# Optimization experiments

Measured on AMD Instinct MI355X. Metric: run time of the kernel, lower is better.

Reference implementation:

```python
import jax, jax.numpy as jnp
import numpy as np

N = 200000   # node_dim
E = 128      # emb_size
B = 4096     # batch of events
H = 20       # hist_len (neighbor_size)
NEG = 5      # neg_size
SIGMA = 1.0
MAXT = 1.0   # max_d_time
INDEX = 4096.0


def setup_inputs() -> dict:
    key = jax.random.key(0)
    ks = jax.random.split(key, 18)
    inp = dict(
        node_features=jax.random.normal(ks[0], (N, E), jnp.float32),
        sources=jax.random.randint(ks[1], (B,), 0, N),
        destinations=jax.random.randint(ks[2], (B,), 0, N),
        e_times=jax.random.uniform(ks[3], (B,), jnp.float32),
        s_h_nodes=jax.random.randint(ks[4], (B, H), 0, N),
        t_h_nodes=jax.random.randint(ks[5], (B, H), 0, N),
        s_h_times=jax.random.uniform(ks[6], (B, H), jnp.float32),
        t_h_times=jax.random.uniform(ks[7], (B, H), jnp.float32),
        s_mask=(jax.random.uniform(ks[8], (B, H)) < 0.9).astype(jnp.float32),
        t_mask=(jax.random.uniform(ks[9], (B, H)) < 0.9).astype(jnp.float32),
        neg_src=jax.random.randint(ks[10], (B * NEG,), 0, N),
        neg_dst=jax.random.randint(ks[11], (B * NEG,), 0, N),
        # MLP: Linear(E,60) -> ReLU -> Linear(60,E)
        W1=jax.random.normal(ks[12], (E, 60), jnp.float32) * 0.05,
        b1=jnp.zeros((60,), jnp.float32),
        W2=jax.random.normal(ks[13], (60, E), jnp.float32) * 0.05,
        b2=jnp.zeros((E,), jnp.float32),
        # GAT params
        W=jax.random.normal(ks[14], (E, E), jnp.float32) * 0.05,
        a=jax.random.normal(ks[15], (2 * E, 1), jnp.float32) * 0.05,
        delta_s_p=jnp.ones((N,), jnp.float32),
        delta_t_p=jnp.ones((N,), jnp.float32),
        gw=jax.random.normal(ks[16], (E, 1), jnp.float32) * 0.05,
        gb=jnp.zeros((1,), jnp.float32),
    )
    return inp


def _forward(node_features, sources, destinations, e_times, s_h_nodes, t_h_nodes,
             s_h_times, t_h_times, s_mask, t_mask, neg_src, neg_dst,
             W1, b1, W2, b2, W, a, delta_s_p, delta_t_p, gw, gb):
    # MLP node embedding
    node_emb = jnp.maximum(node_features @ W1 + b1, 0.0) @ W2 + b2  # [N,E]

    pos0 = node_emb[sources]        # [B,E]
    pos1 = node_emb[destinations]   # [B,E]
    pos = jax.nn.relu(jnp.sum(pos0 * pos1, axis=1))  # [B]

    neg0 = node_emb[neg_src].reshape(B, NEG, E)
    neg1 = node_emb[neg_dst].reshape(B, NEG, E)
    neg_s = jax.nn.relu(jnp.einsum('be,bne->bn', pos0, neg1))
    neg_t = jax.nn.relu(jnp.einsum('be,bne->bn', pos1, neg0))

    # --- computer_similarity (vectorized over hist_len) ---
    et = e_times / MAXT
    d_s = jnp.abs(et[:, None] - s_h_times / MAXT)   # [B,H]
    d_t = jnp.abs(et[:, None] - t_h_times / MAXT)   # [B,H]
    ds = delta_s_p[sources][:, None]                 # [B,1]
    dt = delta_t_p[destinations][:, None]            # [B,1]

    s_h_emb = node_emb[s_h_nodes]   # [B,H,E]
    t_h_emb = node_emb[t_h_nodes]   # [B,H,E]

    a1, a2 = a[:E, 0], a[E:, 0]
    proj_s = pos0 @ W               # [B,E]
    proj_t = pos1 @ W
    proj_sh = jnp.einsum('bhe,ef->bhf', s_h_emb, W)  # [B,H,E]
    proj_th = jnp.einsum('bhe,ef->bhf', t_h_emb, W)

    score_s = (proj_s @ a1)[:, None] + jnp.einsum('bhe,e->bh', proj_sh, a2)
    score_t = (proj_t @ a1)[:, None] + jnp.einsum('bhe,e->bh', proj_th, a2)
    # NOTE: original code uses delta_s for BOTH branches (bug kept for fidelity)
    sim_s = jax.nn.leaky_relu(jnp.exp(-ds * d_s) * score_s, negative_slope=0.2)
    sim_t = jax.nn.leaky_relu(jnp.exp(-ds * d_t) * score_t, negative_slope=0.2)

    att_s = jax.nn.softmax(sim_s, axis=1)   # [B,H]
    att_t = jax.nn.softmax(sim_t, axis=1)

    s_hat = jnp.sum((att_s * s_mask)[:, :, None] * proj_sh, axis=1)  # [B,E]
    t_hat = jnp.sum((att_t * t_mask)[:, :, None] * proj_th, axis=1)

    g_s = s_hat * jnp.exp(-ds * jnp.mean(d_s, axis=1, keepdims=True))
    g_t = t_hat * jnp.exp(-dt * jnp.mean(d_t, axis=1, keepdims=True))
    stacked = jnp.stack([g_s, g_t], axis=1)                  # [B,2,E]
    glogits = jnp.tanh(stacked @ gw + gb)                    # [B,2,1]
    gatt = jax.nn.softmax(glogits, axis=1)[:, :, 0]          # [B,2]
    ga_s, ga_t = gatt[:, 0], gatt[:, 1]

    p_mu = jnp.sum((pos0 - pos1) ** 2, axis=1)                       # [B]
    p_alpha_s = jnp.sum((s_h_emb - pos1[:, None, :]) ** 2, axis=2)   # [B,H]
    p_alpha_t = jnp.sum((t_h_emb - pos0[:, None, :]) ** 2, axis=2)
    p_lambda = (p_mu
                + ga_s * jnp.sum(att_s * p_alpha_s * jnp.exp(ds * d_s) * s_mask, axis=1)
                + ga_t * jnp.sum(att_t * p_alpha_t * jnp.exp(dt * d_t) * t_mask, axis=1))

    n_mu_s = jnp.sum((pos0[:, None, :] - neg1) ** 2, axis=2)  # [B,NEG]
    n_mu_t = jnp.sum((pos1[:, None, :] - neg0) ** 2, axis=2)
    n_alpha_s = jnp.sum((s_h_emb[:, :, None, :] - neg1[:, None, :, :]) ** 2, axis=3)  # [B,H,NEG]
    n_alpha_t = jnp.sum((t_h_emb[:, :, None, :] - neg0[:, None, :, :]) ** 2, axis=3)
    n_lambda_s = n_mu_s + ga_s[:, None] * jnp.sum(
        att_s[:, :, None] * n_alpha_s * jnp.exp(ds * d_s)[:, :, None] * s_mask[:, :, None], axis=1)
    n_lambda_t = n_mu_t + ga_t[:, None] * jnp.sum(
        att_t[:, :, None] * n_alpha_t * jnp.exp(dt * d_t)[:, :, None] * t_mask[:, :, None], axis=1)

    # --- loss ---
    pos_loss = -jnp.log(jax.nn.sigmoid(p_lambda / SIGMA) + 1e-6) * (pos - 1.0) ** 2
    s_neg_loss = -jnp.log(jax.nn.sigmoid(-n_lambda_s / SIGMA) + 1e-6) * neg_s ** 2
    t_neg_loss = -jnp.log(jax.nn.sigmoid(-n_lambda_t / SIGMA) + 1e-6) * neg_t ** 2
    tgsl_loss = pos_loss.sum() / INDEX + (s_neg_loss.sum() + t_neg_loss.sum()) / (INDEX * NEG)

    estimated_weights = pos  # relu(sum(x0*x1)) same as pos
    return tgsl_loss, estimated_weights, node_emb


def reference(node_features, sources, destinations, e_times, s_h_nodes, t_h_nodes,
              s_h_times, t_h_times, s_mask, t_mask, neg_src, neg_dst,
              W1, b1, W2, b2, W, a, delta_s_p, delta_t_p, gw, gb):
    return _forward(node_features, sources, destinations, e_times, s_h_nodes, t_h_nodes,
                    s_h_times, t_h_times, s_mask, t_mask, neg_src, neg_dst,
                    W1, b1, W2, b2, W, a, delta_s_p, delta_t_p, gw, gb)
```

## Files before the change

kernel.cpp:

```cpp
#include <hip/hip_runtime.h>
#include <hip/hip_bf16.h>
#include <math.h>

#define N_NODES 200000
#define E_DIM   128
#define B_EDGES 4096
#define H_NBRS  20
#define NEG_K   5
#define HID     60
#define Z_ROW   (N_NODES + 3)

typedef short bf16x8 __attribute__((ext_vector_type(8)));
typedef float f32x4  __attribute__((ext_vector_type(4)));

#define MFMA(a, b, c) __builtin_amdgcn_mfma_f32_16x16x32_bf16((a), (b), (c), 0, 0, 0)

__device__ __forceinline__ unsigned short f2b(float f) {
  unsigned u = __float_as_uint(f);
  u += 0x7fffu + ((u >> 16) & 1u);
  return (unsigned short)(u >> 16);
}

__device__ __forceinline__ float wave_sum(float v) {
  #pragma unroll
  for (int m = 1; m < 64; m <<= 1) v += __shfl_xor(v, m, 64);
  return v;
}
__device__ __forceinline__ float wave_max(float v) {
  #pragma unroll
  for (int m = 1; m < 64; m <<= 1) v = fmaxf(v, __shfl_xor(v, m, 64));
  return v;
}

__device__ __forceinline__ bf16x8 xfrag(const unsigned short* xS, int m, int kk, int q) {
  int chunk = (kk * 4 + q) ^ ((m & 3) << 2);
  return *(const bf16x8*)(xS + m * 128 + chunk * 8);
}

__global__ __launch_bounds__(1024) void prep_kernel(
    const float* __restrict__ W, const float* __restrict__ a,
    const float* __restrict__ gw, const float* __restrict__ W1,
    const float* __restrict__ W2, unsigned short* __restrict__ w1f,
    unsigned short* __restrict__ w2f, float* __restrict__ wav,
    unsigned short* __restrict__ embH, float* __restrict__ out_loss) {
  __shared__ float wavS[3 * E_DIM];
  const int tid = threadIdx.x;
  const int lane = tid & 63, grp = tid >> 6;
  const int q = lane >> 4, c = lane & 15;

  {
    const int kk = grp >> 2, t = grp & 3;
    const int n = t * 16 + c, k0 = kk * 32 + q * 8;
    unsigned v[4];
    #pragma unroll
    for (int jj = 0; jj < 4; ++jj) {
      unsigned short lo = (n < 60) ? f2b(W1[(k0 + 2 * jj) * 60 + n]) : 0;
      unsigned short hi = (n < 60) ? f2b(W1[(k0 + 2 * jj + 1) * 60 + n]) : 0;
      v[jj] = (unsigned)lo | ((unsigned)hi << 16);
    }
    ((uint4*)w1f)[grp * 64 + lane] = make_uint4(v[0], v[1], v[2], v[3]);
  }
  {
    const int ks = grp >> 3, t = grp & 7;
    const int n = t * 16 + c, k0 = ks * 32 + q * 8;
    unsigned v[4];
    #pragma unroll
    for (int jj = 0; jj < 4; ++jj) {
      int k = k0 + 2 * jj;
      unsigned short lo = (k < 60) ? f2b(W2[k * 128 + n]) : 0;
      unsigned short hi = (k + 1 < 60) ? f2b(W2[(k + 1) * 128 + n]) : 0;
      v[jj] = (unsigned)lo | ((unsigned)hi << 16);
    }
    ((uint4*)w2f)[grp * 64 + lane] = make_uint4(v[0], v[1], v[2], v[3]);
  }
  if (tid < 128) {
    const float* row = W + tid * E_DIM;
    float s1 = 0.f, s2 = 0.f, sg = 0.f;
    for (int f = 0; f < E_DIM; ++f) {
      float w = row[f];
      s1 = fmaf(w, a[f], s1);
      s2 = fmaf(w, a[E_DIM + f], s2);
      sg = fmaf(w, gw[f], sg);
    }
    wav[tid] = s1; wav[E_DIM + tid] = s2; wav[2 * E_DIM + tid] = sg;
    wavS[tid] = s1; wavS[E_DIM + tid] = s2; wavS[2 * E_DIM + tid] = sg;
  }
  __syncthreads();
  if (embH && tid < 512) {
    int r = tid >> 7, col = tid & 127;
    embH[(size_t)(N_NODES + r) * E_DIM + col] = (r < 3) ? f2b(wavS[r * E_DIM + col]) : 0;
  }
  if (tid == 0) *out_loss = 0.f;
}

__global__ __launch_bounds__(256) void mlp_kernel(
    const float* __restrict__ nf, const unsigned short* __restrict__ w1f,
    const unsigned short* __restrict__ w2f, const float* __restrict__ b1,
    const float* __restrict__ b2, float* __restrict__ emb,
    unsigned short* __restrict__ embH) {
  __shared__ unsigned short aS[4][16 * 128];
  __shared__ float cS[4][16 * 68];

  const int tid = threadIdx.x, wave = tid >> 6, lane = tid & 63;
  const int q = lane >> 4, c = lane & 15;
  unsigned short* aw = aS[wave];
  float* cw = cS[wave];
  const size_t R = (size_t)blockIdx.x * 64 + wave * 16;

  #pragma unroll
  for (int it = 0; it < 8; ++it) {
    int v = it * 64 + lane;
    int r = v >> 5, c4 = v & 31;
    float4 x = *(const float4*)(nf + (R + r) * E_DIM + c4 * 4);
    int chunk = c4 >> 1, half = c4 & 1;
    int phys = r * 128 + (((chunk ^ ((r & 3) << 2))) << 3) + (half << 2);
    *(ushort4*)&aw[phys] = make_ushort4(f2b(x.x), f2b(x.y), f2b(x.z), f2b(x.w));
  }

  bf16x8 w1[16];
  #pragma unroll
  for (int g = 0; g < 16; ++g) w1[g] = *(const bf16x8*)(w1f + (g * 64 + lane) * 8);

  f32x4 acc1[4] = {};
  #pragma unroll
  for (int kk = 0; kk < 4; ++kk) {
    bf16x8 av = xfrag(aw, c, kk, q);
    #pragma unroll
    for (int t = 0; t < 4; ++t) acc1[t] = MFMA(av, w1[kk * 4 + t], acc1[t]);
  }
  #pragma unroll
  for (int t = 0; t < 4; ++t) {
    int n = t * 16 + c;
    float bv = (n < 60) ? b1[n] : 0.f;
    #pragma unroll
    for (int i = 0; i < 4; ++i)
      cw[(q * 4 + i) * 68 + n] = fmaxf(acc1[t][i] + bv, 0.f);
  }

  bf16x8 a2[2];
  #pragma unroll
  for (int ks = 0; ks < 2; ++ks) {
    f32x4 r0 = *(const f32x4*)&cw[c * 68 + ks * 32 + q * 8];
    f32x4 r1 = *(const f32x4*)&cw[c * 68 + ks * 32 + q * 8 + 4];
    bf16x8 t8;
    #pragma unroll
    for (int j = 0; j < 4; ++j) {
      t8[j] = (short)f2b(r0[j]);
      t8[4 + j] = (short)f2b(r1[j]);
    }
    a2[ks] = t8;
  }

  bf16x8 w2r[16];
  #pragma unroll
  for (int g = 0; g < 16; ++g) w2r[g] = *(const bf16x8*)(w2f + (g * 64 + lane) * 8);

  f32x4 acc2[8] = {};
  #pragma unroll
  for (int ks = 0; ks < 2; ++ks)
    #pragma unroll
    for (int t = 0; t < 8; ++t) acc2[t] = MFMA(a2[ks], w2r[ks * 8 + t], acc2[t]);

  if (embH) {
    #pragma unroll
    for (int t = 0; t < 8; ++t) {
      int n = t * 16 + c;
      float bv = b2[n];
      #pragma unroll
      for (int i = 0; i < 4; ++i) {
        float val = acc2[t][i] + bv;
        __builtin_nontemporal_store(val, &emb[(R + q * 4 + i) * E_DIM + n]);
        embH[(R + q * 4 + i) * E_DIM + n] = f2b(val);
      }
    }
  } else {
    #pragma unroll
    for (int t = 0; t < 8; ++t) {
      int n = t * 16 + c;
      float bv = b2[n];
      #pragma unroll
      for (int i = 0; i < 4; ++i)
        emb[(R + q * 4 + i) * E_DIM + n] = acc2[t][i] + bv;
    }
  }
}

__global__ __launch_bounds__(256) void edge_kernel(
    const float* __restrict__ emb, const unsigned short* __restrict__ embH,
    const int* __restrict__ sources, const int* __restrict__ destinations,
    const float* __restrict__ e_times,
    const int* __restrict__ s_h_nodes, const int* __restrict__ t_h_nodes,
    const float* __restrict__ s_h_times, const float* __restrict__ t_h_times,
    const float* __restrict__ s_maskp, const float* __restrict__ t_maskp,
    const int* __restrict__ neg_src, const int* __restrict__ neg_dst,
    const float* __restrict__ wav,
    const float* __restrict__ delta_s_p, const float* __restrict__ delta_t_p,
    const float* __restrict__ gbp,
    float* __restrict__ out_loss, float* __restrict__ out_pos) {
  __shared__ unsigned short xS[64 * 128];
  __shared__ float gA[64 * 17];
  __shared__ float diagS[64];
  __shared__ float S[64];
  __shared__ int rows[64];

  const int b = blockIdx.x;
  const int tid = threadIdx.x;
  const int wave = tid >> 6, lane = tid & 63;
  const int q = lane >> 4, c = lane & 15;

  if (tid < 64) {
    int idx = Z_ROW;
    if (tid == 0)       idx = sources[b];
    else if (tid == 1)  idx = destinations[b];
    else if (tid < 7)   idx = neg_src[b * NEG_K + (tid - 2)];
    else if (tid < 12)  idx = neg_dst[b * NEG_K + (tid - 7)];
    else if (tid == 12) idx = N_NODES;
    else if (tid == 13) idx = N_NODES + 1;
    else if (tid == 14) idx = N_NODES + 2;
    else if (tid >= 16 && tid < 36) idx = s_h_nodes[b * H_NBRS + (tid - 16)];
    else if (tid >= 36 && tid < 56) idx = t_h_nodes[b * H_NBRS + (tid - 36)];
    rows[tid] = idx;
  }
  __syncthreads();

  if (embH) {
    #pragma unroll
    for (int it = 0; it < 4; ++it) {
      int v = it * 256 + tid;
      int r = v >> 4, ch = v & 15;
      uint4 u = *(const uint4*)(embH + (size_t)rows[r] * E_DIM + ch * 8);
      int phys = ch ^ ((r & 3) << 2);
      *(uint4*)&xS[r * 128 + phys * 8] = u;
    }
  } else {
    #pragma unroll
    for (int it = 0; it < 8; ++it) {
      int v = it * 256 + tid;
      int r = v >> 5, c4 = v & 31;
      float4 x = make_float4(0.f, 0.f, 0.f, 0.f);
      if (r < 12 || (r >= 16 && r < 56))
        x = *(const float4*)(emb + (size_t)rows[r] * E_DIM + c4 * 4);
      else if (r >= 12 && r < 15)
        x = *(const float4*)(wav + (r - 12) * E_DIM + c4 * 4);
      int chunk = c4 >> 1, half = c4 & 1;
      int phys = r * 128 + ((chunk ^ ((r & 3) << 2)) << 3) + (half << 2);
      *(ushort4*)&xS[phys] = make_ushort4(f2b(x.x), f2b(x.y), f2b(x.z), f2b(x.w));
    }
  }
  __syncthreads();

  {
    f32x4 accA = {0.f, 0.f, 0.f, 0.f};
    f32x4 accB = {0.f, 0.f, 0.f, 0.f};
    #pragma unroll
    for (int kk = 0; kk < 4; ++kk) {
      bf16x8 av = xfrag(xS, wave * 16 + c, kk, q);
      bf16x8 b0 = xfrag(xS, c, kk, q);
      accA = MFMA(av, b0, accA);
      accB = MFMA(av, av, accB);
    }
    #pragma unroll
    for (int i = 0; i < 4; ++i) {
      gA[(wave * 16 + q * 4 + i) * 17 + c] = accA[i];
      if (c == q * 4 + i) diagS[wave * 16 + q * 4 + i] = accB[i];
    }
  }
  __syncthreads();

  const float ds = delta_s_p[rows[0]];
  const float dt = delta_t_p[rows[1]];
  const float et = e_times[b];
  const float gb0 = gbp[0];

  if (wave < 2) {
    const bool is_s = (wave == 0);
    const float dd = is_s ? ds : dt;
    float dval = 0.f, maskv = 0.f, simv = -INFINITY, pav = 0.f, gdot = 0.f;
    if (lane < H_NBRS) {
      int hr = (is_s ? 16 : 36) + lane;
      float ht = is_s ? s_h_times[b * H_NBRS + lane] : t_h_times[b * H_NBRS + lane];
      maskv    = is_s ? s_maskp[b * H_NBRS + lane]   : t_maskp[b * H_NBRS + lane];
      dval = fabsf(et - ht);
      float score = gA[(is_s ? 0 : 1) * 17 + 12] + gA[hr * 17 + 13];
      float x = expf(-ds * dval) * score;
      simv = (x > 0.f) ? x : 0.2f * x;
      int other = is_s ? 1 : 0;
      pav = diagS[hr] + gA[other * 17 + other] - 2.f * gA[hr * 17 + other];
      gdot = gA[hr * 17 + 14];
    }
    float m = wave_max(simv);
    float ev = (lane < H_NBRS) ? expf(simv - m) : 0.f;
    float att = ev / wave_sum(ev);
    float meand = wave_sum(dval) * (1.f / (float)H_NBRS);
    float Eh = expf(dd * dval);
    float cm = att * maskv;
    float P = wave_sum((lane < H_NBRS) ? cm * pav * Eh : 0.f);
    float gsum = wave_sum((lane < H_NBRS) ? cm * gdot : 0.f);
    if (lane < H_NBRS) S[(is_s ? 0 : 20) + lane] = cm * Eh;
    if (lane == 0) {
      S[40 + wave] = P;
      S[42 + wave] = tanhf(expf(-dd * meand) * gsum + gb0);
    }
  }
  __syncthreads();

  if (wave == 0) {
    float gls = S[42], glt = S[43];
    float mg = fmaxf(gls, glt);
    float eg_s = expf(gls - mg), eg_t = expf(glt - mg);
    float inv = 1.f / (eg_s + eg_t);
    float ga_s = eg_s * inv, ga_t = eg_t * inv;

    float nl = 0.f;
    if (lane < NEG_K) {
      int nr = 7 + lane;
      float diag_n = gA[nr * 17 + nr];
      float n_mu = gA[0] + diag_n - 2.f * gA[0 * 17 + nr];
      float acc = 0.f;
      #pragma unroll
      for (int h = 0; h < H_NBRS; ++h)
        acc = fmaf(S[h], diagS[16 + h] + diag_n - 2.f * gA[(16 + h) * 17 + nr], acc);
      float nls = n_mu + ga_s * acc;
      float ns = fmaxf(gA[0 * 17 + nr], 0.f);
      nl = -logf(1.f / (1.f + expf(nls)) + 1e-6f) * ns * ns;
    } else if (lane < 2 * NEG_K) {
      int n = lane - NEG_K;
      int nr = 2 + n;
      float diag_n = gA[nr * 17 + nr];
      float n_mu = gA[1 * 17 + 1] + diag_n - 2.f * gA[1 * 17 + nr];
      float acc = 0.f;
      #pragma unroll
      for (int h = 0; h < H_NBRS; ++h)
        acc = fmaf(S[20 + h], diagS[36 + h] + diag_n - 2.f * gA[(36 + h) * 17 + nr], acc);
      float nlt = n_mu + ga_t * acc;
      float ns = fmaxf(gA[1 * 17 + nr], 0.f);
      nl = -logf(1.f / (1.f + expf(nlt)) + 1e-6f) * ns * ns;
    }
    float nsum = wave_sum(nl);
    if (lane == 0) {
      float p_mu = gA[0] + gA[1 * 17 + 1] - 2.f * gA[1];
      float p_lambda = p_mu + ga_s * S[40] + ga_t * S[41];
      float pos = fmaxf(gA[1], 0.f);
      float pl = -logf(1.f / (1.f + expf(-p_lambda)) + 1e-6f) * (pos - 1.f) * (pos - 1.f);
      atomicAdd(out_loss, pl * (1.f / 4096.f) + nsum * (1.f / (4096.f * 5.f)));
      out_pos[b] = pos;
    }
  }
}

extern "C" void kernel_launch(void* const* d_in, const int* in_sizes, int n_in,
                              void* d_out, int out_size, void* d_ws, size_t ws_size,
                              hipStream_t stream) {
  const float* nf           = (const float*)d_in[0];
  const int*   sources      = (const int*)d_in[1];
  const int*   destinations = (const int*)d_in[2];
  const float* e_times      = (const float*)d_in[3];
  const int*   s_h_nodes    = (const int*)d_in[4];
  const int*   t_h_nodes    = (const int*)d_in[5];
  const float* s_h_times    = (const float*)d_in[6];
  const float* t_h_times    = (const float*)d_in[7];
  const float* s_mask       = (const float*)d_in[8];
  const float* t_mask       = (const float*)d_in[9];
  const int*   neg_src      = (const int*)d_in[10];
  const int*   neg_dst      = (const int*)d_in[11];
  const float* W1           = (const float*)d_in[12];
  const float* b1           = (const float*)d_in[13];
  const float* W2           = (const float*)d_in[14];
  const float* b2           = (const float*)d_in[15];
  const float* W            = (const float*)d_in[16];
  const float* a            = (const float*)d_in[17];
  const float* delta_s_p    = (const float*)d_in[18];
  const float* delta_t_p    = (const float*)d_in[19];
  const float* gw           = (const float*)d_in[20];
  const float* gb           = (const float*)d_in[21];

  float* out      = (float*)d_out;
  float* out_loss = out;
  float* out_pos  = out + 1;
  float* emb      = out + 1 + B_EDGES;

  size_t embH_bytes = (size_t)(N_NODES + 4) * E_DIM * sizeof(unsigned short);
  bool useH = ws_size >= embH_bytes + 2 * 16384 + 3 * E_DIM * sizeof(float) + 256;
  char* p = (char*)d_ws;
  unsigned short* embH = nullptr;
  if (useH) { embH = (unsigned short*)p; p += embH_bytes; }
  unsigned short* w1f = (unsigned short*)p; p += 16384;
  unsigned short* w2f = (unsigned short*)p; p += 16384;
  float*          wav = (float*)p;

  prep_kernel<<<1, 1024, 0, stream>>>(W, a, gw, W1, W2, w1f, w2f, wav, embH, out_loss);
  mlp_kernel<<<N_NODES / 64, 256, 0, stream>>>(nf, w1f, w2f, b1, b2, emb, embH);
  edge_kernel<<<B_EDGES, 256, 0, stream>>>(emb, embH, sources, destinations, e_times,
      s_h_nodes, t_h_nodes, s_h_times, t_h_times, s_mask, t_mask, neg_src, neg_dst,
      wav, delta_s_p, delta_t_p, gb, out_loss, out_pos);
}
```

Measured before the change: 376.3 us.

## Load MLP input fragments directly to registers and stage output through LDS

```diff
diff --git a/kernel.cpp b/kernel.cpp
--- a/kernel.cpp
+++ b/kernel.cpp
@@ -98,23 +98,19 @@
     const unsigned short* __restrict__ w2f, const float* __restrict__ b1,
     const float* __restrict__ b2, float* __restrict__ emb,
     unsigned short* __restrict__ embH) {
-  __shared__ unsigned short aS[4][16 * 128];
-  __shared__ float cS[4][16 * 68];
+  __shared__ float smem[4][16 * 68];
 
   const int tid = threadIdx.x, wave = tid >> 6, lane = tid & 63;
   const int q = lane >> 4, c = lane & 15;
-  unsigned short* aw = aS[wave];
-  float* cw = cS[wave];
+  float* cw = smem[wave];
   const size_t R = (size_t)blockIdx.x * 64 + wave * 16;
 
-  #pragma unroll
-  for (int it = 0; it < 8; ++it) {
-    int v = it * 64 + lane;
-    int r = v >> 5, c4 = v & 31;
-    float4 x = *(const float4*)(nf + (R + r) * E_DIM + c4 * 4);
-    int chunk = c4 >> 1, half = c4 & 1;
-    int phys = r * 128 + (((chunk ^ ((r & 3) << 2))) << 3) + (half << 2);
-    *(ushort4*)&aw[phys] = make_ushort4(f2b(x.x), f2b(x.y), f2b(x.z), f2b(x.w));
+  const float* arow = nf + (R + c) * E_DIM + q * 8;
+  float4 a0[4], a1[4];
+  #pragma unroll
+  for (int kk = 0; kk < 4; ++kk) {
+    a0[kk] = *(const float4*)(arow + kk * 32);
+    a1[kk] = *(const float4*)(arow + kk * 32 + 4);
   }
 
   bf16x8 w1[16];
@@ -124,7 +120,11 @@
   f32x4 acc1[4] = {};
   #pragma unroll
   for (int kk = 0; kk < 4; ++kk) {
-    bf16x8 av = xfrag(aw, c, kk, q);
+    bf16x8 av;
+    av[0] = (short)f2b(a0[kk].x); av[1] = (short)f2b(a0[kk].y);
+    av[2] = (short)f2b(a0[kk].z); av[3] = (short)f2b(a0[kk].w);
+    av[4] = (short)f2b(a1[kk].x); av[5] = (short)f2b(a1[kk].y);
+    av[6] = (short)f2b(a1[kk].z); av[7] = (short)f2b(a1[kk].w);
     #pragma unroll
     for (int t = 0; t < 4; ++t) acc1[t] = MFMA(av, w1[kk * 4 + t], acc1[t]);
   }
@@ -161,26 +161,30 @@
     #pragma unroll
     for (int t = 0; t < 8; ++t) acc2[t] = MFMA(a2[ks], w2r[ks * 8 + t], acc2[t]);
 
-  if (embH) {
-    #pragma unroll
-    for (int t = 0; t < 8; ++t) {
+  #pragma unroll
+  for (int h = 0; h < 2; ++h) {
+    #pragma unroll
+    for (int t = 0; t < 4; ++t) {
       int n = t * 16 + c;
-      float bv = b2[n];
-      #pragma unroll
-      for (int i = 0; i < 4; ++i) {
-        float val = acc2[t][i] + bv;
-        __builtin_nontemporal_store(val, &emb[(R + q * 4 + i) * E_DIM + n]);
-        embH[(R + q * 4 + i) * E_DIM + n] = f2b(val);
-      }
-    }
-  } else {
-    #pragma unroll
-    for (int t = 0; t < 8; ++t) {
-      int n = t * 16 + c;
-      float bv = b2[n];
+      float bv = b2[h * 64 + n];
       #pragma unroll
       for (int i = 0; i < 4; ++i)
-        emb[(R + q * 4 + i) * E_DIM + n] = acc2[t][i] + bv;
+        cw[(q * 4 + i) * 68 + n] = acc2[h * 4 + t][i] + bv;
+    }
+    #pragma unroll
+    for (int it = 0; it < 4; ++it) {
+      int v = it * 64 + lane;
+      int r = v >> 4, c4 = v & 15;
+      f32x4 x = *(const f32x4*)&cw[r * 68 + c4 * 4];
+      float* dst = emb + (R + r) * E_DIM + h * 64 + c4 * 4;
+      __builtin_nontemporal_store(x[0], dst + 0);
+      __builtin_nontemporal_store(x[1], dst + 1);
+      __builtin_nontemporal_store(x[2], dst + 2);
+      __builtin_nontemporal_store(x[3], dst + 3);
+      if (embH) {
+        ushort4 pk = make_ushort4(f2b(x[0]), f2b(x[1]), f2b(x[2]), f2b(x[3]));
+        *(ushort4*)(embH + (R + r) * E_DIM + h * 64 + c4 * 4) = pk;
+      }
     }
   }
 }
```

New measurement: 337.4 us. -10.3%, faster.
